# Performance work log

Measured on AMD Instinct MI355X. Metric: run time of the kernel, lower is better.

## Reference

```python
import jax, jax.numpy as jnp
import numpy as np

N, E, D, H = 50000, 400000, 128, 256


def setup_inputs() -> dict:
    key = jax.random.key(0)
    ks = jax.random.split(key, 16)
    s = 0.02
    inp = {
        "x": jax.random.normal(ks[0], (N, D), dtype=jnp.float32),
        "edge_index": jax.random.randint(ks[1], (2, E), 0, N, dtype=jnp.int64),
        "steps": 1,
        # encoder MLP: Linear(D->H), Linear(H->H), relu after each
        "enc_w1": jax.random.normal(ks[2], (H, D), dtype=jnp.float32) * s,
        "enc_b1": jnp.zeros((H,), dtype=jnp.float32),
        "enc_w2": jax.random.normal(ks[3], (H, H), dtype=jnp.float32) * s,
        "enc_b2": jnp.zeros((H,), dtype=jnp.float32),
        # GeneralConv lin_msg (root_weight=False, bias=True)
        "msg_w": jax.random.normal(ks[4], (H, H), dtype=jnp.float32) * s,
        "msg_b": jnp.zeros((H,), dtype=jnp.float32),
        # decoder MLP: Linear(2H->H) relu, Linear(H->D) tanh
        "dec_w1": jax.random.normal(ks[5], (H, 2 * H), dtype=jnp.float32) * s,
        "dec_b1": jnp.zeros((H,), dtype=jnp.float32),
        "dec_w2": jax.random.normal(ks[6], (D, H), dtype=jnp.float32) * s,
        "dec_b2": jnp.zeros((D,), dtype=jnp.float32),
    }
    return inp


def reference(x, edge_index, steps, enc_w1, enc_b1, enc_w2, enc_b2,
              msg_w, msg_b, dec_w1, dec_b1, dec_w2, dec_b2):
    src = edge_index[0]
    dst = edge_index[1]
    n = x.shape[0]
    for _ in range(steps):  # steps is a small static python int
        # encoder MLP (batch_norm=False, dropout=0, relu + relu)
        h = jax.nn.relu(x @ enc_w1.T + enc_b1)
        h = jax.nn.relu(h @ enc_w2.T + enc_b2)
        # GeneralConv: message = lin_msg(x_j); aggr='add'; no root weight
        # lin_msg is edge-independent -> transform on nodes, then gather/scatter
        m = h @ msg_w.T + msg_b                      # [N, H]
        out = jax.ops.segment_sum(m[src], dst, num_segments=n)  # [N, H]
        # decoder on cat(out, h): relu then tanh
        d = jax.nn.relu(jnp.concatenate([out, h], axis=-1) @ dec_w1.T + dec_b1)
        x = jnp.tanh(d @ dec_w2.T + dec_b2)
    return x
```

## Files before the change

### kernel.cpp

```cpp
#include <hip/hip_runtime.h>
#include <cmath>


typedef __attribute__((ext_vector_type(8))) short  short8;
typedef __attribute__((ext_vector_type(4))) float  f32x4;
typedef __attribute__((ext_vector_type(4))) unsigned short us4;

typedef unsigned short u16;
typedef unsigned int   u32;

static __device__ __forceinline__ u16 f2bf(float f) {
    u32 u = __float_as_uint(f);
    u = (u + 0x7FFFu + ((u >> 16) & 1u)) >> 16;
    return (u16)u;
}
static __device__ __forceinline__ float bf2f(u16 h) {
    return __uint_as_float(((u32)h) << 16);
}

static __device__ __forceinline__ void g2l16(const void* g, void* l) {
    __builtin_amdgcn_global_load_lds(
        (const __attribute__((address_space(1))) u32*)g,
        (__attribute__((address_space(3))) u32*)l, 16, 0, 0);
}

static __device__ __forceinline__ short8 cvt8(const float* p) {
    short8 r;
#pragma unroll
    for (int e = 0; e < 8; e++) r[e] = (short)f2bf(p[e]);
    return r;
}

__global__ __launch_bounds__(512, 2) void enc_fused(
    const float* __restrict__ x, const u16* __restrict__ w1,
    const float* __restrict__ b1, const u16* __restrict__ w2,
    const float* __restrict__ b2, const u16* __restrict__ wm,
    const float* __restrict__ bm, u16* __restrict__ hout,
    u16* __restrict__ mout, const int N)
{
    __shared__ u16 Ws[256 * 32];
    __shared__ u16 hL[8][64 * 32];
    float* AsF = (float*)&hL[0][0];

    const int t    = threadIdx.x;
    const int r0   = blockIdx.x * 64;
    const int wave = t >> 6;
    const int lane = t & 63;
    const int n    = lane & 15;
    const int q    = lane >> 4;
    const int wc   = wave * 32;
    const int lrow = lane >> 2;
    const int qofs = (lane & 3) * 8;

    const int axrow = min(r0 + wave * 8 + (lane >> 3), N - 1);
    const float* xp = x + (size_t)axrow * 128 + (lane & 7) * 4;

    const int wrA = wave * 16 + lrow;
    const int wrB = (wave + 8) * 16 + lrow;

    f32x4 acc[4][2];
#pragma unroll
    for (int i = 0; i < 4; i++)
#pragma unroll
        for (int j = 0; j < 2; j++) acc[i][j] = (f32x4)0.0f;

    for (int c = 0; c < 4; c++) {
        __syncthreads();
        g2l16(xp + c * 32, &AsF[wave * 256]);
        g2l16(w1 + (size_t)wrA * 128 + c * 32 + qofs, &Ws[wave * 512]);
        g2l16(w1 + (size_t)wrB * 128 + c * 32 + qofs, &Ws[(wave + 8) * 512]);
        __syncthreads();
        short8 af[4], bf[2];
#pragma unroll
        for (int i = 0; i < 4; i++)
            af[i] = cvt8(&AsF[(i * 16 + n) * 32 + q * 8]);
#pragma unroll
        for (int j = 0; j < 2; j++)
            bf[j] = *reinterpret_cast<const short8*>(&Ws[(wc + j * 16 + n) * 32 + q * 8]);
#pragma unroll
        for (int i = 0; i < 4; i++)
#pragma unroll
            for (int j = 0; j < 2; j++)
                acc[i][j] = __builtin_amdgcn_mfma_f32_16x16x32_bf16(
                    af[i], bf[j], acc[i][j], 0, 0, 0);
    }
    __syncthreads();
    {
        float bv[2];
#pragma unroll
        for (int j = 0; j < 2; j++) bv[j] = b1[wc + j * 16 + n];
#pragma unroll
        for (int i = 0; i < 4; i++)
#pragma unroll
            for (int reg = 0; reg < 4; reg++) {
                const int row = i * 16 + q * 4 + reg;
#pragma unroll
                for (int j = 0; j < 2; j++) {
                    const float v = fmaxf(acc[i][j][reg] + bv[j], 0.0f);
                    hL[wave][row * 32 + j * 16 + n] = f2bf(v);
                }
            }
    }

#pragma unroll
    for (int i = 0; i < 4; i++)
#pragma unroll
        for (int j = 0; j < 2; j++) acc[i][j] = (f32x4)0.0f;
    for (int c = 0; c < 8; c++) {
        __syncthreads();
        g2l16(w2 + (size_t)wrA * 256 + c * 32 + qofs, &Ws[wave * 512]);
        g2l16(w2 + (size_t)wrB * 256 + c * 32 + qofs, &Ws[(wave + 8) * 512]);
        __syncthreads();
        short8 af[4], bf[2];
#pragma unroll
        for (int i = 0; i < 4; i++)
            af[i] = *reinterpret_cast<const short8*>(&hL[c][(i * 16 + n) * 32 + q * 8]);
#pragma unroll
        for (int j = 0; j < 2; j++)
            bf[j] = *reinterpret_cast<const short8*>(&Ws[(wc + j * 16 + n) * 32 + q * 8]);
#pragma unroll
        for (int i = 0; i < 4; i++)
#pragma unroll
            for (int j = 0; j < 2; j++)
                acc[i][j] = __builtin_amdgcn_mfma_f32_16x16x32_bf16(
                    af[i], bf[j], acc[i][j], 0, 0, 0);
    }
    {
        float bv[2];
#pragma unroll
        for (int j = 0; j < 2; j++) bv[j] = b2[wc + j * 16 + n];
#pragma unroll
        for (int i = 0; i < 4; i++)
#pragma unroll
            for (int reg = 0; reg < 4; reg++) {
                const int row = r0 + i * 16 + q * 4 + reg;
                if (row < N) {
#pragma unroll
                    for (int j = 0; j < 2; j++) {
                        const float v = fmaxf(acc[i][j][reg] + bv[j], 0.0f);
                        hout[(size_t)row * 256 + wc + j * 16 + n] = f2bf(v);
                    }
                }
            }
        __syncthreads();
#pragma unroll
        for (int i = 0; i < 4; i++)
#pragma unroll
            for (int reg = 0; reg < 4; reg++) {
                const int row = i * 16 + q * 4 + reg;
#pragma unroll
                for (int j = 0; j < 2; j++) {
                    const float v = fmaxf(acc[i][j][reg] + bv[j], 0.0f);
                    hL[wave][row * 32 + j * 16 + n] = f2bf(v);
                }
            }
    }

#pragma unroll
    for (int i = 0; i < 4; i++)
#pragma unroll
        for (int j = 0; j < 2; j++) acc[i][j] = (f32x4)0.0f;
    for (int c = 0; c < 8; c++) {
        __syncthreads();
        g2l16(wm + (size_t)wrA * 256 + c * 32 + qofs, &Ws[wave * 512]);
        g2l16(wm + (size_t)wrB * 256 + c * 32 + qofs, &Ws[(wave + 8) * 512]);
        __syncthreads();
        short8 af[4], bf[2];
#pragma unroll
        for (int i = 0; i < 4; i++)
            af[i] = *reinterpret_cast<const short8*>(&hL[c][(i * 16 + n) * 32 + q * 8]);
#pragma unroll
        for (int j = 0; j < 2; j++)
            bf[j] = *reinterpret_cast<const short8*>(&Ws[(wc + j * 16 + n) * 32 + q * 8]);
#pragma unroll
        for (int i = 0; i < 4; i++)
#pragma unroll
            for (int j = 0; j < 2; j++)
                acc[i][j] = __builtin_amdgcn_mfma_f32_16x16x32_bf16(
                    af[i], bf[j], acc[i][j], 0, 0, 0);
    }
    {
        float bv[2];
#pragma unroll
        for (int j = 0; j < 2; j++) bv[j] = bm[wc + j * 16 + n];
#pragma unroll
        for (int i = 0; i < 4; i++)
#pragma unroll
            for (int reg = 0; reg < 4; reg++) {
                const int row = r0 + i * 16 + q * 4 + reg;
                if (row < N) {
#pragma unroll
                    for (int j = 0; j < 2; j++)
                        mout[(size_t)row * 256 + wc + j * 16 + n] =
                            f2bf(acc[i][j][reg] + bv[j]);
                }
            }
    }
}

__global__ __launch_bounds__(512, 2) void dec_fused(
    const u16* __restrict__ aggr, const u16* __restrict__ h,
    const u16* __restrict__ wd1, const float* __restrict__ bd1,
    const u16* __restrict__ wd2, const float* __restrict__ bd2,
    float* __restrict__ out, const int N)
{
    __shared__ u16 As[64 * 32];
    __shared__ u16 Ws[256 * 32];
    __shared__ u16 dL[8][64 * 32];

    const int t    = threadIdx.x;
    const int r0   = blockIdx.x * 64;
    const int wave = t >> 6;
    const int lane = t & 63;
    const int n    = lane & 15;
    const int q    = lane >> 4;
    const int wc   = wave * 32;
    const int lrow = lane >> 2;
    const int qofs = (lane & 3) * 8;

    const int arow = min(r0 + wave * 16 + lrow, N - 1);
    const u16* ap0 = aggr + (size_t)arow * 256 + qofs;
    const u16* ap1 = h    + (size_t)arow * 256 + qofs;
    const int wrA = wave * 16 + lrow;
    const int wrB = (wave + 8) * 16 + lrow;

    f32x4 acc[4][2];
#pragma unroll
    for (int i = 0; i < 4; i++)
#pragma unroll
        for (int j = 0; j < 2; j++) acc[i][j] = (f32x4)0.0f;

    for (int kc = 0; kc < 512; kc += 32) {
        __syncthreads();
        if (wave < 4) {
            if (kc < 256) g2l16(ap0 + kc, &As[wave * 512]);
            else          g2l16(ap1 + (kc - 256), &As[wave * 512]);
        }
        g2l16(wd1 + (size_t)wrA * 512 + kc + qofs, &Ws[wave * 512]);
        g2l16(wd1 + (size_t)wrB * 512 + kc + qofs, &Ws[(wave + 8) * 512]);
        __syncthreads();
        short8 af[4], bf[2];
#pragma unroll
        for (int i = 0; i < 4; i++)
            af[i] = *reinterpret_cast<const short8*>(&As[(i * 16 + n) * 32 + q * 8]);
#pragma unroll
        for (int j = 0; j < 2; j++)
            bf[j] = *reinterpret_cast<const short8*>(&Ws[(wc + j * 16 + n) * 32 + q * 8]);
#pragma unroll
        for (int i = 0; i < 4; i++)
#pragma unroll
            for (int j = 0; j < 2; j++)
                acc[i][j] = __builtin_amdgcn_mfma_f32_16x16x32_bf16(
                    af[i], bf[j], acc[i][j], 0, 0, 0);
    }
    {
        float bv[2];
#pragma unroll
        for (int j = 0; j < 2; j++) bv[j] = bd1[wc + j * 16 + n];
#pragma unroll
        for (int i = 0; i < 4; i++)
#pragma unroll
            for (int reg = 0; reg < 4; reg++) {
                const int row = i * 16 + q * 4 + reg;
#pragma unroll
                for (int j = 0; j < 2; j++) {
                    const float v = fmaxf(acc[i][j][reg] + bv[j], 0.0f);
                    dL[wave][row * 32 + j * 16 + n] = f2bf(v);
                }
            }
    }

    f32x4 acc2[4];
#pragma unroll
    for (int i = 0; i < 4; i++) acc2[i] = (f32x4)0.0f;
    const int wc2 = wave * 16;
    for (int c = 0; c < 8; c++) {
        __syncthreads();
        g2l16(wd2 + (size_t)(wave * 16 + lrow) * 256 + c * 32 + qofs,
              &Ws[wave * 512]);
        __syncthreads();
        short8 af[4], bf;
#pragma unroll
        for (int i = 0; i < 4; i++)
            af[i] = *reinterpret_cast<const short8*>(&dL[c][(i * 16 + n) * 32 + q * 8]);
        bf = *reinterpret_cast<const short8*>(&Ws[(wave * 16 + n) * 32 + q * 8]);
#pragma unroll
        for (int i = 0; i < 4; i++)
            acc2[i] = __builtin_amdgcn_mfma_f32_16x16x32_bf16(
                af[i], bf, acc2[i], 0, 0, 0);
    }
    {
        const float bv = bd2[wc2 + n];
#pragma unroll
        for (int i = 0; i < 4; i++)
#pragma unroll
            for (int reg = 0; reg < 4; reg++) {
                const int row = r0 + i * 16 + q * 4 + reg;
                if (row < N)
                    out[(size_t)row * 128 + wc2 + n] = tanhf(acc2[i][reg] + bv);
            }
    }
}

__global__ __launch_bounds__(256) void cvt6_kernel(
    const float* s0, const float* s1, const float* s2, const float* s3,
    const float* s4,
    u16* d0, u16* d1, u16* d2, u16* d3, u16* d4,
    int* __restrict__ zp,
    int n0, int n1, int n2, int n3, int n4, int nz)
{
    const int i = blockIdx.x * 256 + threadIdx.x;
    if (blockIdx.y == 5) {
        if (i < nz) zp[i] = 0;
        return;
    }
    const float* s; u16* d; int nq;
    switch (blockIdx.y) {
        case 0: s = s0; d = d0; nq = n0; break;
        case 1: s = s1; d = d1; nq = n1; break;
        case 2: s = s2; d = d2; nq = n2; break;
        case 3: s = s3; d = d3; nq = n3; break;
        default: s = s4; d = d4; nq = n4; break;
    }
    if (i < nq) {
        const float4 v = reinterpret_cast<const float4*>(s)[i];
        us4 o = { f2bf(v.x), f2bf(v.y), f2bf(v.z), f2bf(v.w) };
        reinterpret_cast<us4*>(d)[i] = o;
    }
}

__global__ __launch_bounds__(256) void fill_kernel(
    const int* __restrict__ ei, int* __restrict__ cursor,
    int* __restrict__ bucket, const int E, const int Nn)
{
    const int e = blockIdx.x * 256 + threadIdx.x;
    if (e < E) {
        const int src = ei[e];
        const int dst = ei[(size_t)E + e];
        if ((unsigned)dst < (unsigned)Nn) {
            const int pos = atomicAdd(&cursor[dst], 1);
            if (pos < 64) bucket[(size_t)dst * 64 + pos] = src;
        }
    }
}

__global__ __launch_bounds__(256) void gather_sum_kernel(
    const u16* __restrict__ m, const int* __restrict__ bucket,
    const int* __restrict__ cursor, u16* __restrict__ outa, const int Nn)
{
    const int wave = (int)((blockIdx.x * 256u + threadIdx.x) >> 6);
    const int lane = threadIdx.x & 63;
    if (wave >= Nn) return;
    const int cnt = min(cursor[wave], 64);
    const int* bl = bucket + (size_t)wave * 64;
    float a0 = 0.f, a1 = 0.f, a2 = 0.f, a3 = 0.f;
    for (int base = 0; base < cnt; base += 8) {
        int sidx[8];
#pragma unroll
        for (int u = 0; u < 8; u++)
            sidx[u] = (base + u < cnt) ? bl[base + u] : -1;
        us4 v[8];
#pragma unroll
        for (int u = 0; u < 8; u++) {
            const int s = ((unsigned)sidx[u] < (unsigned)Nn) ? sidx[u] : 0;
            v[u] = *reinterpret_cast<const us4*>(&m[(size_t)s * 256 + lane * 4]);
        }
#pragma unroll
        for (int u = 0; u < 8; u++) {
            if ((unsigned)sidx[u] < (unsigned)Nn) {
                a0 += bf2f(v[u].x); a1 += bf2f(v[u].y);
                a2 += bf2f(v[u].z); a3 += bf2f(v[u].w);
            }
        }
    }
    us4 o = { f2bf(a0), f2bf(a1), f2bf(a2), f2bf(a3) };
    *reinterpret_cast<us4*>(&outa[(size_t)wave * 256 + lane * 4]) = o;
}

extern "C" void kernel_launch(void* const* d_in, const int* in_sizes, int n_in,
                              void* d_out, int out_size, void* d_ws, size_t ws_size,
                              hipStream_t stream)
{
    const float* x      = (const float*)d_in[0];
    const int*   ei     = (const int*)d_in[1];
    const float* enc_w1 = (const float*)d_in[3];
    const float* enc_b1 = (const float*)d_in[4];
    const float* enc_w2 = (const float*)d_in[5];
    const float* enc_b2 = (const float*)d_in[6];
    const float* msg_w  = (const float*)d_in[7];
    const float* msg_b  = (const float*)d_in[8];
    const float* dec_w1 = (const float*)d_in[9];
    const float* dec_b1 = (const float*)d_in[10];
    const float* dec_w2 = (const float*)d_in[11];
    const float* dec_b2 = (const float*)d_in[12];

    const int N = 50000, D = 128, H = 256;
    const int E = in_sizes[1] / 2;

    u16* h    = (u16*)d_ws;
    u16* m    = h    + (size_t)N * H;
    u16* aggr = m    + (size_t)N * H;
    u16* w1   = aggr + (size_t)N * H;
    u16* w2   = w1 + 256 * 128;
    u16* wm   = w2 + 256 * 256;
    u16* wd1  = wm + 256 * 256;
    u16* wd2  = wd1 + 256 * 512;
    int* cursor = (int*)(wd2 + 128 * 256);
    int* bucket = cursor + N;

    const dim3 blk(256);
    const dim3 blk512(512);
    const int nb64 = (N + 63) / 64;
    const int cvtx = (N + 255) / 256;

    cvt6_kernel<<<dim3(cvtx, 6), blk, 0, stream>>>(
        enc_w1, enc_w2, msg_w, dec_w1, dec_w2,
        w1, w2, wm, wd1, wd2, cursor,
        256 * 128 / 4, 256 * 256 / 4, 256 * 256 / 4,
        256 * 512 / 4, 128 * 256 / 4, N);

    fill_kernel<<<dim3((E + 255) / 256), blk, 0, stream>>>(
        ei, cursor, bucket, E, N);

    enc_fused<<<dim3(nb64), blk512, 0, stream>>>(
        x, w1, enc_b1, w2, enc_b2, wm, msg_b, h, m, N);

    gather_sum_kernel<<<dim3((N * 64 + 255) / 256), blk, 0, stream>>>(
        m, bucket, cursor, aggr, N);

    dec_fused<<<dim3(nb64), blk512, 0, stream>>>(
        aggr, h, wd1, dec_b1, wd2, dec_b2, (float*)d_out, N);
}
```

Measured before the change: 238.6 us.

## Load weights directly from global into registers and preload activation tiles once

Weight tiles are no longer staged through LDS. Each wave reads its bf16 weight fragments straight from global memory into registers, relying on L2/cache reuse across blocks. The whole 64-row activation tile is loaded into LDS up front, which removes the per-k-chunk pair of barriers and cuts LDS to 32KB. Launch bounds rise to 4 blocks per CU for more occupancy. The trade-off is more global/L2 traffic for weights and possible register pressure under the tighter bound.

```diff
diff --git a/kernel.cpp b/kernel.cpp
--- a/kernel.cpp
+++ b/kernel.cpp
@@ -24,6 +24,10 @@
         (__attribute__((address_space(3))) u32*)l, 16, 0, 0);
 }
 
+static __device__ __forceinline__ short8 ld8(const u16* p) {
+    return *reinterpret_cast<const short8*>(p);
+}
+
 static __device__ __forceinline__ short8 cvt8(const float* p) {
     short8 r;
 #pragma unroll
@@ -31,16 +35,176 @@
     return r;
 }
 
-__global__ __launch_bounds__(512, 2) void enc_fused(
+__global__ __launch_bounds__(512, 4) void enc_fused(
     const float* __restrict__ x, const u16* __restrict__ w1,
     const float* __restrict__ b1, const u16* __restrict__ w2,
     const float* __restrict__ b2, const u16* __restrict__ wm,
     const float* __restrict__ bm, u16* __restrict__ hout,
     u16* __restrict__ mout, const int N)
 {
-    __shared__ u16 Ws[256 * 32];
-    __shared__ u16 hL[8][64 * 32];
-    float* AsF = (float*)&hL[0][0];
+    __shared__ u16 hL[16384];
+    float* AsF = (float*)hL;
+
+    const int t    = threadIdx.x;
+    const int r0   = blockIdx.x * 64;
+    const int wave = t >> 6;
+    const int lane = t & 63;
+    const int n    = lane & 15;
+    const int q    = lane >> 4;
+    const int wc   = wave * 32;
+
+#pragma unroll
+    for (int s = 0; s < 4; s++) {
+        const int g  = wave + s * 8;
+        const int c  = g >> 3, rg = g & 7;
+        const int grow = rg * 8 + (lane >> 3);
+        const int arow = min(r0 + grow, N - 1);
+        g2l16(x + (size_t)arow * 128 + c * 32 + (lane & 7) * 4, &AsF[g * 256]);
+    }
+    __syncthreads();
+
+    f32x4 acc[4][2];
+#pragma unroll
+    for (int i = 0; i < 4; i++)
+#pragma unroll
+        for (int j = 0; j < 2; j++) acc[i][j] = (f32x4)0.0f;
+
+#pragma unroll
+    for (int c = 0; c < 4; c++) {
+        short8 bf[2];
+#pragma unroll
+        for (int j = 0; j < 2; j++)
+            bf[j] = ld8(w1 + (size_t)(wc + j * 16 + n) * 128 + c * 32 + q * 8);
+        short8 af[4];
+#pragma unroll
+        for (int i = 0; i < 4; i++)
+            af[i] = cvt8(&AsF[c * 2048 + (i * 16 + n) * 32 + q * 8]);
+#pragma unroll
+        for (int i = 0; i < 4; i++)
+#pragma unroll
+            for (int j = 0; j < 2; j++)
+                acc[i][j] = __builtin_amdgcn_mfma_f32_16x16x32_bf16(
+                    af[i], bf[j], acc[i][j], 0, 0, 0);
+    }
+    __syncthreads();
+    {
+        float bv[2];
+#pragma unroll
+        for (int j = 0; j < 2; j++) bv[j] = b1[wc + j * 16 + n];
+#pragma unroll
+        for (int i = 0; i < 4; i++)
+#pragma unroll
+            for (int reg = 0; reg < 4; reg++) {
+                const int row = i * 16 + q * 4 + reg;
+#pragma unroll
+                for (int j = 0; j < 2; j++) {
+                    const float v = fmaxf(acc[i][j][reg] + bv[j], 0.0f);
+                    hL[wave * 2048 + row * 32 + j * 16 + n] = f2bf(v);
+                }
+            }
+    }
+    __syncthreads();
+
+#pragma unroll
+    for (int i = 0; i < 4; i++)
+#pragma unroll
+        for (int j = 0; j < 2; j++) acc[i][j] = (f32x4)0.0f;
+#pragma unroll
+    for (int c = 0; c < 8; c++) {
+        short8 bf[2];
+#pragma unroll
+        for (int j = 0; j < 2; j++)
+            bf[j] = ld8(w2 + (size_t)(wc + j * 16 + n) * 256 + c * 32 + q * 8);
+        short8 af[4];
+#pragma unroll
+        for (int i = 0; i < 4; i++)
+            af[i] = ld8(&hL[c * 2048 + (i * 16 + n) * 32 + q * 8]);
+#pragma unroll
+        for (int i = 0; i < 4; i++)
+#pragma unroll
+            for (int j = 0; j < 2; j++)
+                acc[i][j] = __builtin_amdgcn_mfma_f32_16x16x32_bf16(
+                    af[i], bf[j], acc[i][j], 0, 0, 0);
+    }
+    {
+        float bv[2];
+#pragma unroll
+        for (int j = 0; j < 2; j++) bv[j] = b2[wc + j * 16 + n];
+#pragma unroll
+        for (int i = 0; i < 4; i++)
+#pragma unroll
+            for (int reg = 0; reg < 4; reg++) {
+                const int row = r0 + i * 16 + q * 4 + reg;
+                if (row < N) {
+#pragma unroll
+                    for (int j = 0; j < 2; j++) {
+                        const float v = fmaxf(acc[i][j][reg] + bv[j], 0.0f);
+                        hout[(size_t)row * 256 + wc + j * 16 + n] = f2bf(v);
+                    }
+                }
+            }
+        __syncthreads();
+#pragma unroll
+        for (int i = 0; i < 4; i++)
+#pragma unroll
+            for (int reg = 0; reg < 4; reg++) {
+                const int row = i * 16 + q * 4 + reg;
+#pragma unroll
+                for (int j = 0; j < 2; j++) {
+                    const float v = fmaxf(acc[i][j][reg] + bv[j], 0.0f);
+                    hL[wave * 2048 + row * 32 + j * 16 + n] = f2bf(v);
+                }
+            }
+    }
+    __syncthreads();
+
+#pragma unroll
+    for (int i = 0; i < 4; i++)
+#pragma unroll
+        for (int j = 0; j < 2; j++) acc[i][j] = (f32x4)0.0f;
+#pragma unroll
+    for (int c = 0; c < 8; c++) {
+        short8 bf[2];
+#pragma unroll
+        for (int j = 0; j < 2; j++)
+            bf[j] = ld8(wm + (size_t)(wc + j * 16 + n) * 256 + c * 32 + q * 8);
+        short8 af[4];
+#pragma unroll
+        for (int i = 0; i < 4; i++)
+            af[i] = ld8(&hL[c * 2048 + (i * 16 + n) * 32 + q * 8]);
+#pragma unroll
+        for (int i = 0; i < 4; i++)
+#pragma unroll
+            for (int j = 0; j < 2; j++)
+                acc[i][j] = __builtin_amdgcn_mfma_f32_16x16x32_bf16(
+                    af[i], bf[j], acc[i][j], 0, 0, 0);
+    }
+    {
+        float bv[2];
+#pragma unroll
+        for (int j = 0; j < 2; j++) bv[j] = bm[wc + j * 16 + n];
+#pragma unroll
+        for (int i = 0; i < 4; i++)
+#pragma unroll
+            for (int reg = 0; reg < 4; reg++) {
+                const int row = r0 + i * 16 + q * 4 + reg;
+                if (row < N) {
+#pragma unroll
+                    for (int j = 0; j < 2; j++)
+                        mout[(size_t)row * 256 + wc + j * 16 + n] =
+                            f2bf(acc[i][j][reg] + bv[j]);
+                }
+            }
+    }
+}
+
+__global__ __launch_bounds__(512, 4) void dec_fused(
+    const u16* __restrict__ aggr, const u16* __restrict__ h,
+    const u16* __restrict__ wd1, const float* __restrict__ bd1,
+    const u16* __restrict__ wd2, const float* __restrict__ bd2,
+    float* __restrict__ out, const int N)
+{
+    __shared__ u16 AL[16384];
 
     const int t    = threadIdx.x;
     const int r0   = blockIdx.x * 64;
@@ -52,11 +216,15 @@
     const int lrow = lane >> 2;
     const int qofs = (lane & 3) * 8;
 
-    const int axrow = min(r0 + wave * 8 + (lane >> 3), N - 1);
-    const float* xp = x + (size_t)axrow * 128 + (lane & 7) * 4;
-
-    const int wrA = wave * 16 + lrow;
-    const int wrB = (wave + 8) * 16 + lrow;
+#pragma unroll
+    for (int s = 0; s < 4; s++) {
+        const int g  = wave + s * 8;
+        const int c  = g >> 2, rg = g & 3;
+        const int grow = rg * 16 + lrow;
+        const int arow = min(r0 + grow, N - 1);
+        g2l16(aggr + (size_t)arow * 256 + c * 32 + qofs, &AL[g * 512]);
+    }
+    __syncthreads();
 
     f32x4 acc[4][2];
 #pragma unroll
@@ -64,19 +232,16 @@
 #pragma unroll
         for (int j = 0; j < 2; j++) acc[i][j] = (f32x4)0.0f;
 
-    for (int c = 0; c < 4; c++) {
-        __syncthreads();
-        g2l16(xp + c * 32, &AsF[wave * 256]);
-        g2l16(w1 + (size_t)wrA * 128 + c * 32 + qofs, &Ws[wave * 512]);
-        g2l16(w1 + (size_t)wrB * 128 + c * 32 + qofs, &Ws[(wave + 8) * 512]);
-        __syncthreads();
-        short8 af[4], bf[2];
-#pragma unroll
-        for (int i = 0; i < 4; i++)
-            af[i] = cvt8(&AsF[(i * 16 + n) * 32 + q * 8]);
+#pragma unroll
+    for (int c = 0; c < 8; c++) {
+        short8 bf[2];
 #pragma unroll
         for (int j = 0; j < 2; j++)
-            bf[j] = *reinterpret_cast<const short8*>(&Ws[(wc + j * 16 + n) * 32 + q * 8]);
+            bf[j] = ld8(wd1 + (size_t)(wc + j * 16 + n) * 512 + c * 32 + q * 8);
+        short8 af[4];
+#pragma unroll
+        for (int i = 0; i < 4; i++)
+            af[i] = ld8(&AL[c * 2048 + (i * 16 + n) * 32 + q * 8]);
 #pragma unroll
         for (int i = 0; i < 4; i++)
 #pragma unroll
@@ -85,39 +250,26 @@
                     af[i], bf[j], acc[i][j], 0, 0, 0);
     }
     __syncthreads();
-    {
-        float bv[2];
-#pragma unroll
-        for (int j = 0; j < 2; j++) bv[j] = b1[wc + j * 16 + n];
-#pragma unroll
-        for (int i = 0; i < 4; i++)
-#pragma unroll
-            for (int reg = 0; reg < 4; reg++) {
-                const int row = i * 16 + q * 4 + reg;
-#pragma unroll
-                for (int j = 0; j < 2; j++) {
-                    const float v = fmaxf(acc[i][j][reg] + bv[j], 0.0f);
-                    hL[wave][row * 32 + j * 16 + n] = f2bf(v);
-                }
-            }
-    }
-
-#pragma unroll
-    for (int i = 0; i < 4; i++)
-#pragma unroll
-        for (int j = 0; j < 2; j++) acc[i][j] = (f32x4)0.0f;
-    for (int c = 0; c < 8; c++) {
-        __syncthreads();
-        g2l16(w2 + (size_t)wrA * 256 + c * 32 + qofs, &Ws[wave * 512]);
-        g2l16(w2 + (size_t)wrB * 256 + c * 32 + qofs, &Ws[(wave + 8) * 512]);
-        __syncthreads();
-        short8 af[4], bf[2];
-#pragma unroll
-        for (int i = 0; i < 4; i++)
-            af[i] = *reinterpret_cast<const short8*>(&hL[c][(i * 16 + n) * 32 + q * 8]);
+#pragma unroll
+    for (int s = 0; s < 4; s++) {
+        const int g  = wave + s * 8;
+        const int c  = g >> 2, rg = g & 3;
+        const int grow = rg * 16 + lrow;
+        const int arow = min(r0 + grow, N - 1);
+        g2l16(h + (size_t)arow * 256 + c * 32 + qofs, &AL[g * 512]);
+    }
+    __syncthreads();
+
+#pragma unroll
+    for (int c = 8; c < 16; c++) {
+        short8 bf[2];
 #pragma unroll
         for (int j = 0; j < 2; j++)
-            bf[j] = *reinterpret_cast<const short8*>(&Ws[(wc + j * 16 + n) * 32 + q * 8]);
+            bf[j] = ld8(wd1 + (size_t)(wc + j * 16 + n) * 512 + c * 32 + q * 8);
+        short8 af[4];
+#pragma unroll
+        for (int i = 0; i < 4; i++)
+            af[i] = ld8(&AL[(c - 8) * 2048 + (i * 16 + n) * 32 + q * 8]);
 #pragma unroll
         for (int i = 0; i < 4; i++)
 #pragma unroll
@@ -125,24 +277,11 @@
                 acc[i][j] = __builtin_amdgcn_mfma_f32_16x16x32_bf16(
                     af[i], bf[j], acc[i][j], 0, 0, 0);
     }
+    __syncthreads();
     {
         float bv[2];
 #pragma unroll
-        for (int j = 0; j < 2; j++) bv[j] = b2[wc + j * 16 + n];
-#pragma unroll
-        for (int i = 0; i < 4; i++)
-#pragma unroll
-            for (int reg = 0; reg < 4; reg++) {
-                const int row = r0 + i * 16 + q * 4 + reg;
-                if (row < N) {
-#pragma unroll
-                    for (int j = 0; j < 2; j++) {
-                        const float v = fmaxf(acc[i][j][reg] + bv[j], 0.0f);
-                        hout[(size_t)row * 256 + wc + j * 16 + n] = f2bf(v);
-                    }
-                }
-            }
-        __syncthreads();
+        for (int j = 0; j < 2; j++) bv[j] = bd1[wc + j * 16 + n];
 #pragma unroll
         for (int i = 0; i < 4; i++)
 #pragma unroll
@@ -151,139 +290,23 @@
 #pragma unroll
                 for (int j = 0; j < 2; j++) {
                     const float v = fmaxf(acc[i][j][reg] + bv[j], 0.0f);
-                    hL[wave][row * 32 + j * 16 + n] = f2bf(v);
+                    AL[wave * 2048 + row * 32 + j * 16 + n] = f2bf(v);
                 }
             }
     }
-
-#pragma unroll
-    for (int i = 0; i < 4; i++)
-#pragma unroll
-        for (int j = 0; j < 2; j++) acc[i][j] = (f32x4)0.0f;
-    for (int c = 0; c < 8; c++) {
-        __syncthreads();
-        g2l16(wm + (size_t)wrA * 256 + c * 32 + qofs, &Ws[wave * 512]);
-        g2l16(wm + (size_t)wrB * 256 + c * 32 + qofs, &Ws[(wave + 8) * 512]);
-        __syncthreads();
-        short8 af[4], bf[2];
-#pragma unroll
-        for (int i = 0; i < 4; i++)
-            af[i] = *reinterpret_cast<const short8*>(&hL[c][(i * 16 + n) * 32 + q * 8]);
-#pragma unroll
-        for (int j = 0; j < 2; j++)
-            bf[j] = *reinterpret_cast<const short8*>(&Ws[(wc + j * 16 + n) * 32 + q * 8]);
-#pragma unroll
-        for (int i = 0; i < 4; i++)
-#pragma unroll
-            for (int j = 0; j < 2; j++)
-                acc[i][j] = __builtin_amdgcn_mfma_f32_16x16x32_bf16(
-                    af[i], bf[j], acc[i][j], 0, 0, 0);
-    }
-    {
-        float bv[2];
-#pragma unroll
-        for (int j = 0; j < 2; j++) bv[j] = bm[wc + j * 16 + n];
-#pragma unroll
-        for (int i = 0; i < 4; i++)
-#pragma unroll
-            for (int reg = 0; reg < 4; reg++) {
-                const int row = r0 + i * 16 + q * 4 + reg;
-                if (row < N) {
-#pragma unroll
-                    for (int j = 0; j < 2; j++)
-                        mout[(size_t)row * 256 + wc + j * 16 + n] =
-                            f2bf(acc[i][j][reg] + bv[j]);
-                }
-            }
-    }
-}
-
-__global__ __launch_bounds__(512, 2) void dec_fused(
-    const u16* __restrict__ aggr, const u16* __restrict__ h,
-    const u16* __restrict__ wd1, const float* __restrict__ bd1,
-    const u16* __restrict__ wd2, const float* __restrict__ bd2,
-    float* __restrict__ out, const int N)
-{
-    __shared__ u16 As[64 * 32];
-    __shared__ u16 Ws[256 * 32];
-    __shared__ u16 dL[8][64 * 32];
-
-    const int t    = threadIdx.x;
-    const int r0   = blockIdx.x * 64;
-    const int wave = t >> 6;
-    const int lane = t & 63;
-    const int n    = lane & 15;
-    const int q    = lane >> 4;
-    const int wc   = wave * 32;
-    const int lrow = lane >> 2;
-    const int qofs = (lane & 3) * 8;
-
-    const int arow = min(r0 + wave * 16 + lrow, N - 1);
-    const u16* ap0 = aggr + (size_t)arow * 256 + qofs;
-    const u16* ap1 = h    + (size_t)arow * 256 + qofs;
-    const int wrA = wave * 16 + lrow;
-    const int wrB = (wave + 8) * 16 + lrow;
-
-    f32x4 acc[4][2];
-#pragma unroll
-    for (int i = 0; i < 4; i++)
-#pragma unroll
-        for (int j = 0; j < 2; j++) acc[i][j] = (f32x4)0.0f;
-
-    for (int kc = 0; kc < 512; kc += 32) {
-        __syncthreads();
-        if (wave < 4) {
-            if (kc < 256) g2l16(ap0 + kc, &As[wave * 512]);
-            else          g2l16(ap1 + (kc - 256), &As[wave * 512]);
-        }
-        g2l16(wd1 + (size_t)wrA * 512 + kc + qofs, &Ws[wave * 512]);
-        g2l16(wd1 + (size_t)wrB * 512 + kc + qofs, &Ws[(wave + 8) * 512]);
-        __syncthreads();
-        short8 af[4], bf[2];
-#pragma unroll
-        for (int i = 0; i < 4; i++)
-            af[i] = *reinterpret_cast<const short8*>(&As[(i * 16 + n) * 32 + q * 8]);
-#pragma unroll
-        for (int j = 0; j < 2; j++)
-            bf[j] = *reinterpret_cast<const short8*>(&Ws[(wc + j * 16 + n) * 32 + q * 8]);
-#pragma unroll
-        for (int i = 0; i < 4; i++)
-#pragma unroll
-            for (int j = 0; j < 2; j++)
-                acc[i][j] = __builtin_amdgcn_mfma_f32_16x16x32_bf16(
-                    af[i], bf[j], acc[i][j], 0, 0, 0);
-    }
-    {
-        float bv[2];
-#pragma unroll
-        for (int j = 0; j < 2; j++) bv[j] = bd1[wc + j * 16 + n];
-#pragma unroll
-        for (int i = 0; i < 4; i++)
-#pragma unroll
-            for (int reg = 0; reg < 4; reg++) {
-                const int row = i * 16 + q * 4 + reg;
-#pragma unroll
-                for (int j = 0; j < 2; j++) {
-                    const float v = fmaxf(acc[i][j][reg] + bv[j], 0.0f);
-                    dL[wave][row * 32 + j * 16 + n] = f2bf(v);
-                }
-            }
-    }
+    __syncthreads();
 
     f32x4 acc2[4];
 #pragma unroll
     for (int i = 0; i < 4; i++) acc2[i] = (f32x4)0.0f;
     const int wc2 = wave * 16;
+#pragma unroll
     for (int c = 0; c < 8; c++) {
-        __syncthreads();
-        g2l16(wd2 + (size_t)(wave * 16 + lrow) * 256 + c * 32 + qofs,
-              &Ws[wave * 512]);
-        __syncthreads();
-        short8 af[4], bf;
-#pragma unroll
-        for (int i = 0; i < 4; i++)
-            af[i] = *reinterpret_cast<const short8*>(&dL[c][(i * 16 + n) * 32 + q * 8]);
-        bf = *reinterpret_cast<const short8*>(&Ws[(wave * 16 + n) * 32 + q * 8]);
+        short8 bf = ld8(wd2 + (size_t)(wc2 + n) * 256 + c * 32 + q * 8);
+        short8 af[4];
+#pragma unroll
+        for (int i = 0; i < 4; i++)
+            af[i] = ld8(&AL[c * 2048 + (i * 16 + n) * 32 + q * 8]);
 #pragma unroll
         for (int i = 0; i < 4; i++)
             acc2[i] = __builtin_amdgcn_mfma_f32_16x16x32_bf16(
```

Measured after the change: 252.6 us. +5.8%, slower.
